# Kernel tuning notes

Measured on AMD Instinct MI355X. Metric: run time of the kernel, lower is better.

Reference implementation:

```python
import jax, jax.numpy as jnp
import numpy as np

B, T, C = 8, 2048, 1024
HEAD_SIZE = 64
HEAD_NUM = 0
NUM_HEADS = 16


def setup_inputs() -> dict:
    key = jax.random.key(0)
    k1, k2, k3, k4 = jax.random.split(key, 4)
    x = jax.random.normal(k1, (B, T, C), dtype=jnp.float32)
    s = C ** -0.5  # Linear init scale
    Wq = jax.random.normal(k2, (C, HEAD_SIZE), dtype=jnp.float32) * s
    Wk = jax.random.normal(k3, (C, HEAD_SIZE), dtype=jnp.float32) * s
    Wv = jax.random.normal(k4, (C, HEAD_SIZE), dtype=jnp.float32) * s
    return {"x": x, "Wq": Wq, "Wk": Wk, "Wv": Wv}


def reference(x, Wq, Wk, Wv):
    # single head of self-attention with ALiBi bias + causal mask (dropout in eval mode = identity)
    q = x @ Wq  # [B,T,H]
    k = x @ Wk  # [B,T,H]
    v = x @ Wv  # [B,T,H]
    scale = jnp.float32(HEAD_SIZE) ** -0.5
    t = jnp.arange(T)
    # base_bias[i,j] = j - i, scaled by per-head ALiBi slope
    slope = 2.0 ** (-8.0 * (HEAD_NUM + 1) / NUM_HEADS)
    m = (t[None, :] - t[:, None]).astype(jnp.float32) * slope  # [T,T]
    # note: bias is added BEFORE the 1/sqrt(d) scaling, as in the original
    scores = (jnp.einsum('bqh,bkh->bqk', q, k) + m) * scale  # [B,T,T]
    causal = t[None, :] <= t[:, None]  # [T,T] lower-triangular
    scores = jnp.where(causal, scores, -jnp.inf)
    attn = jax.nn.softmax(scores, axis=-1)
    out = jnp.einsum('bqk,bkh->bqh', attn, v)  # [B,T,H]
    return out
```

## Files before the change

### kernel.cpp

```cpp
#include <hip/hip_runtime.h>
#include <hip/hip_bf16.h>
#include <math.h>

#define B_ 8
#define T_ 2048
#define C_ 1024
#define H_ 64
#define M_ (B_*T_)

typedef __attribute__((ext_vector_type(8))) short bf16x8;
typedef __attribute__((ext_vector_type(4))) float floatx4;

static __device__ __forceinline__ unsigned short f2bf(float f) {
    union { float f; unsigned u; } v; v.f = f;
    unsigned r = v.u + 0x7fffu + ((v.u >> 16) & 1u);
    return (unsigned short)(r >> 16);
}
static __device__ __forceinline__ unsigned short f2bf_fast(float f) {
    union { float f; unsigned u; } v; v.f = f;
    return (unsigned short)((v.u + 0x8000u) >> 16);
}
static __device__ __forceinline__ unsigned pk2h(float lo, float hi) {
    union { float f; unsigned u; } a, b; a.f = lo; b.f = hi;
    return __builtin_amdgcn_perm(b.u + 0x8000u, a.u + 0x8000u, 0x07060302u);
}
static __device__ __forceinline__ bf16x8 cvt8(float4 f0, float4 f1) {
    union { uint4 u; bf16x8 v; } r;
    r.u.x = pk2h(f0.x, f0.y); r.u.y = pk2h(f0.z, f0.w);
    r.u.z = pk2h(f1.x, f1.y); r.u.w = pk2h(f1.z, f1.w);
    return r.v;
}

#define MFMA(a,b,c) __builtin_amdgcn_mfma_f32_16x16x32_bf16((a),(b),(c),0,0,0)

__global__ __launch_bounds__(256) void wprep_kernel(
    const float* __restrict__ Wq, const float* __restrict__ Wk,
    const float* __restrict__ Wv, unsigned short* __restrict__ wt2)
{
    const int f    = blockIdx.x * 256 + threadIdx.x;
    const int nt   = f >> 11;
    const int kc   = (f >> 6) & 31;
    const int lane = f & 63;
    const int l15  = lane & 15, quad = lane >> 4;
    const int col  = nt * 16 + l15;
    const float* W = (col < 64) ? Wq : ((col < 128) ? Wk : Wv);
    const int   cw = col & 63;
    const float sc = (col < 64) ? 0.125f : 1.0f;
    unsigned short o[8];
    #pragma unroll
    for (int j = 0; j < 8; j++) {
        const int kk = kc * 32 + quad * 8 + j;
        o[j] = f2bf(W[(size_t)kk * 64 + cw] * sc);
    }
    *(uint4*)&wt2[(size_t)f * 8] = *(const uint4*)o;
}

__global__ __launch_bounds__(256) void qkv_kernel(
    const float* __restrict__ x, const unsigned short* __restrict__ wt2,
    unsigned short* __restrict__ qo, unsigned short* __restrict__ ko,
    unsigned short* __restrict__ vo)
{
    __shared__ __align__(16) unsigned short smem[64 * 200];
    #define XS_(buf) (smem + (buf) * 4608)

    const int t    = threadIdx.x;
    const int w    = t >> 6;
    const int lane = t & 63;
    const int l15  = lane & 15;
    const int quad = lane >> 4;
    const int r0   = blockIdx.x * 64;

    const int srow = t >> 2;
    const int g0   = t & 3;
    const float* xrow = x + (size_t)(r0 + srow) * C_;

    const unsigned short* wb = wt2 + (size_t)(w * 3) * 32 * 512 + lane * 8;

    floatx4 acc[4][3];
    #pragma unroll
    for (int mt = 0; mt < 4; mt++)
        #pragma unroll
        for (int nt = 0; nt < 3; nt++) acc[mt][nt] = (floatx4)(0.0f);

    float4 xA[4], xB[4];
    bf16x8 wcur[6], wnxt[6];

    #pragma unroll
    for (int j = 0; j < 2; j++) {
        const int g = g0 + 4 * j;
        xA[2*j+0] = *(const float4*)(xrow + g * 8);
        xA[2*j+1] = *(const float4*)(xrow + g * 8 + 4);
        xB[2*j+0] = *(const float4*)(xrow + 64 + g * 8);
        xB[2*j+1] = *(const float4*)(xrow + 64 + g * 8 + 4);
    }
    #pragma unroll
    for (int nt = 0; nt < 3; nt++)
        #pragma unroll
        for (int ks = 0; ks < 2; ks++)
            wcur[nt * 2 + ks] = *(const bf16x8*)(wb + (size_t)(nt * 32 + ks) * 512);
    #pragma unroll
    for (int j = 0; j < 2; j++) {
        const int g = g0 + 4 * j;
        *(bf16x8*)(XS_(0) + srow * 72 + g * 8) = cvt8(xA[2*j], xA[2*j+1]);
    }
    __syncthreads();

    #define QSTEP(c, Xcur, Xnext, buf)                                         \
    {                                                                          \
        if ((c) < 14) {                                                        \
            const int k2 = ((c) + 2) * 64;                                     \
            _Pragma("unroll")                                                  \
            for (int j = 0; j < 2; j++) {                                      \
                const int g = g0 + 4 * j;                                      \
                Xcur[2*j+0] = *(const float4*)(xrow + k2 + g * 8);             \
                Xcur[2*j+1] = *(const float4*)(xrow + k2 + g * 8 + 4);         \
            }                                                                  \
        }                                                                      \
        if ((c) < 15) {                                                        \
            _Pragma("unroll")                                                  \
            for (int nt = 0; nt < 3; nt++)                                     \
                _Pragma("unroll")                                              \
                for (int ks = 0; ks < 2; ks++)                                 \
                    wnxt[nt * 2 + ks] = *(const bf16x8*)                       \
                        (wb + (size_t)(nt * 32 + 2 * ((c) + 1) + ks) * 512);   \
        }                                                                      \
        _Pragma("unroll")                                                      \
        for (int ks = 0; ks < 2; ks++) {                                       \
            bf16x8 af[4];                                                      \
            _Pragma("unroll")                                                  \
            for (int mt = 0; mt < 4; mt++)                                     \
                af[mt] = *(const bf16x8*)                                      \
                    (XS_(buf) + (mt * 16 + l15) * 72 + ks * 32 + quad * 8);    \
            _Pragma("unroll")                                                  \
            for (int mt = 0; mt < 4; mt++)                                     \
                _Pragma("unroll")                                              \
                for (int nt = 0; nt < 3; nt++)                                 \
                    acc[mt][nt] = MFMA(af[mt], wcur[nt * 2 + ks], acc[mt][nt]);\
        }                                                                      \
        if ((c) < 15) {                                                        \
            _Pragma("unroll")                                                  \
            for (int j = 0; j < 2; j++) {                                      \
                const int g = g0 + 4 * j;                                      \
                *(bf16x8*)(XS_((buf) ^ 1) + srow * 72 + g * 8)                 \
                    = cvt8(Xnext[2*j], Xnext[2*j+1]);                          \
            }                                                                  \
            _Pragma("unroll")                                                  \
            for (int i = 0; i < 6; i++) wcur[i] = wnxt[i];                     \
        }                                                                      \
        __syncthreads();                                                       \
    }

    for (int cc = 0; cc < 16; cc += 2) {
        QSTEP(cc,     xA, xB, 0)
        QSTEP(cc + 1, xB, xA, 1)
    }
    #undef QSTEP

    #pragma unroll
    for (int mt = 0; mt < 4; mt++)
        #pragma unroll
        for (int nt = 0; nt < 3; nt++) {
            const int col = w * 48 + nt * 16 + l15;
            #pragma unroll
            for (int r = 0; r < 4; r++)
                smem[(mt * 16 + quad * 4 + r) * 200 + col] = f2bf(acc[mt][nt][r]);
        }
    __syncthreads();

    {
        #pragma unroll
        for (int i = 0; i < 2; i++) {
            const int fo  = t + i * 256;
            const int row = fo >> 3;
            const int oct = fo & 7;
            *(uint4*)&qo[(size_t)(r0 + row) * 64 + oct * 8] =
                *(const uint4*)&smem[row * 200 + oct * 8];
            *(uint4*)&ko[(size_t)(r0 + row) * 64 + oct * 8] =
                *(const uint4*)&smem[row * 200 + 64 + oct * 8];
        }
    }
    {
        const int h = t >> 2, ts = (t & 3) * 16;
        const int bb = r0 >> 11, tt = r0 & 2047;
        unsigned short tmp[16];
        #pragma unroll
        for (int j = 0; j < 16; j++) tmp[j] = smem[(ts + j) * 200 + 128 + h];
        #pragma unroll
        for (int j = 0; j < 2; j++)
            *(uint4*)&vo[((size_t)bb * 64 + h) * 2048 + tt + ts + j * 8] =
                *(uint4*)&tmp[j * 8];
    }
    #undef XS_
}

__global__ __launch_bounds__(256, 2) void attn_kernel(
    const unsigned short* __restrict__ q,
    const unsigned short* __restrict__ k,
    const unsigned short* __restrict__ vT,
    float* __restrict__ out)
{
    __shared__ __align__(16) unsigned char smem[32768 + 1024];
    unsigned short* pT  = (unsigned short*)smem;
    float*          Omg = (float*)smem;
    float*          mlg = (float*)(smem + 32768);

    const int t    = threadIdx.x;
    const int w    = t >> 6;
    const int lane = t & 63;
    const int l15  = lane & 15;
    const int quad = lane >> 4;
    const int b    = blockIdx.x & 7;
    const int qt   = 63 - (blockIdx.x >> 3);
    const int q0   = qt * 32;
    const size_t kb = (size_t)b * T_ * 64;

    bf16x8 qf[2][2];
    #pragma unroll
    for (int rt = 0; rt < 2; rt++)
        #pragma unroll
        for (int ks = 0; ks < 2; ks++)
            qf[rt][ks] = *(const bf16x8*)
                &q[kb + (size_t)(q0 + rt * 16 + l15) * 64 + ks * 32 + quad * 8];

    floatx4 O[2][4];
    float mrow[2][4], lrow[2][4], igb[2][4];
    const float bs = 0.088388347648318447f;
    #pragma unroll
    for (int rt = 0; rt < 2; rt++) {
        #pragma unroll
        for (int nt = 0; nt < 4; nt++) O[rt][nt] = (floatx4)(0.0f);
        #pragma unroll
        for (int r = 0; r < 4; r++) {
            mrow[rt][r] = -INFINITY; lrow[rt][r] = 0.0f;
            igb[rt][r] = (float)(q0 + rt * 16 + quad * 4 + r) * bs;
        }
    }

    const int nsteps = (q0 + 32 + 63) >> 6;
    const int ns4    = (nsteps + 3) >> 2;
    const int sBeg   = w * ns4;
    const int sEnd   = min(sBeg + ns4, nsteps);
    unsigned short* pw = pT + w * 32 * 72;

    bf16x8 kf[4][2], vf[4][2];
    #define LOADK(dK, jj0)                                                     \
        { _Pragma("unroll")                                                    \
          for (int nt = 0; nt < 4; nt++)                                       \
              _Pragma("unroll")                                                \
              for (int ks = 0; ks < 2; ks++)                                   \
                  dK[nt][ks] = *(const bf16x8*)                                \
                      &k[kb + (size_t)((jj0) + nt*16 + l15)*64 + ks*32 + quad*8]; }
    #define LOADV(dV, jj0)                                                     \
        { _Pragma("unroll")                                                    \
          for (int nt = 0; nt < 4; nt++)                                       \
              _Pragma("unroll")                                                \
              for (int ks = 0; ks < 2; ks++)                                   \
                  dV[nt][ks] = *(const bf16x8*)                                \
                      &vT[((size_t)b*64 + nt*16 + l15)*2048 + (jj0) + ks*32 + quad*8]; }

    if (sBeg < sEnd) LOADK(kf, sBeg * 64)

    for (int s = sBeg; s < sEnd; s++) {
        const int j0 = s * 64;

        floatx4 sc[2][4];
        #pragma unroll
        for (int rt = 0; rt < 2; rt++)
            #pragma unroll
            for (int nt = 0; nt < 4; nt++) {
                floatx4 z = (floatx4)(0.0f);
                z = MFMA(qf[rt][0], kf[nt][0], z);
                z = MFMA(qf[rt][1], kf[nt][1], z);
                sc[rt][nt] = z;
            }

        LOADV(vf, j0)
        bf16x8 kf2[4][2];
        const bool more = (s + 1 < sEnd);
        if (more) LOADK(kf2, (s + 1) * 64)

        const float jbase = (float)(j0 + l15) * bs;
        #pragma unroll
        for (int rt = 0; rt < 2; rt++)
            #pragma unroll
            for (int r = 0; r < 4; r++) {
                const int   ig = q0 + rt * 16 + quad * 4 + r;
                const float c0 = jbase - igb[rt][r];
                float xv[4];
                float mloc = -INFINITY;
                #pragma unroll
                for (int nt = 0; nt < 4; nt++) {
                    const int j = j0 + nt * 16 + l15;
                    float v2 = (sc[rt][nt][r] + c0) + (float)(nt * 16) * bs;
                    if (j > ig) v2 = -INFINITY;
                    xv[nt] = v2;
                    mloc = fmaxf(mloc, v2);
                }
                #pragma unroll
                for (int off = 1; off < 16; off <<= 1)
                    mloc = fmaxf(mloc, __shfl_xor(mloc, off));
                const float mnew = fmaxf(mrow[rt][r], mloc);
                const float mq   = (mnew == -INFINITY) ? 0.0f : mnew;
                const float alpha = __expf(mrow[rt][r] - mq);
                mrow[rt][r] = mnew;
                float ps = 0.0f;
                #pragma unroll
                for (int nt = 0; nt < 4; nt++) {
                    const float p = __expf(xv[nt] - mq);
                    ps += p;
                    pw[(rt * 16 + quad * 4 + r) * 72 + nt * 16 + l15] = f2bf_fast(p);
                }
                lrow[rt][r] = lrow[rt][r] * alpha + ps;
                #pragma unroll
                for (int nt = 0; nt < 4; nt++) O[rt][nt][r] *= alpha;
            }

        #pragma unroll
        for (int rt = 0; rt < 2; rt++) {
            const bf16x8 pf0 = *(const bf16x8*)&pw[(rt * 16 + l15) * 72 + quad * 8];
            const bf16x8 pf1 = *(const bf16x8*)&pw[(rt * 16 + l15) * 72 + 32 + quad * 8];
            #pragma unroll
            for (int nt = 0; nt < 4; nt++) {
                O[rt][nt] = MFMA(pf0, vf[nt][0], O[rt][nt]);
                O[rt][nt] = MFMA(pf1, vf[nt][1], O[rt][nt]);
            }
        }

        if (more) {
            #pragma unroll
            for (int nt = 0; nt < 4; nt++)
                #pragma unroll
                for (int ks = 0; ks < 2; ks++)
                    kf[nt][ks] = kf2[nt][ks];
        }
    }
    #undef LOADK
    #undef LOADV

    #pragma unroll
    for (int rt = 0; rt < 2; rt++)
        #pragma unroll
        for (int r = 0; r < 4; r++)
            #pragma unroll
            for (int off = 1; off < 16; off <<= 1)
                lrow[rt][r] += __shfl_xor(lrow[rt][r], off);

    __syncthreads();

    #pragma unroll
    for (int rt = 0; rt < 2; rt++)
        #pragma unroll
        for (int nt = 0; nt < 4; nt++)
            #pragma unroll
            for (int r = 0; r < 4; r++)
                Omg[w * 2048 + (rt * 16 + quad * 4 + r) * 64 + nt * 16 + l15]
                    = O[rt][nt][r];
    if (l15 == 0) {
        #pragma unroll
        for (int rt = 0; rt < 2; rt++)
            #pragma unroll
            for (int r = 0; r < 4; r++) {
                mlg[w * 64 + rt * 16 + quad * 4 + r]      = mrow[rt][r];
                mlg[w * 64 + 32 + rt * 16 + quad * 4 + r] = lrow[rt][r];
            }
    }
    __syncthreads();

    {
        const int row = t >> 3;
        const int hq  = (t & 7) << 3;
        float mstar = -INFINITY;
        #pragma unroll
        for (int w2 = 0; w2 < 4; w2++)
            mstar = fmaxf(mstar, mlg[w2 * 64 + row]);
        floatx4 oa0 = (floatx4)(0.0f), oa1 = (floatx4)(0.0f);
        float lsum = 0.0f;
        #pragma unroll
        for (int w2 = 0; w2 < 4; w2++) {
            const float wg = __expf(mlg[w2 * 64 + row] - mstar);
            lsum += wg * mlg[w2 * 64 + 32 + row];
            oa0 += wg * *(const floatx4*)&Omg[w2 * 2048 + row * 64 + hq];
            oa1 += wg * *(const floatx4*)&Omg[w2 * 2048 + row * 64 + hq + 4];
        }
        const float inv = 1.0f / lsum;
        *(floatx4*)&out[kb + (size_t)(q0 + row) * 64 + hq]     = oa0 * inv;
        *(floatx4*)&out[kb + (size_t)(q0 + row) * 64 + hq + 4] = oa1 * inv;
    }
}

extern "C" void kernel_launch(void* const* d_in, const int* in_sizes, int n_in,
                              void* d_out, int out_size, void* d_ws, size_t ws_size,
                              hipStream_t stream) {
    (void)in_sizes; (void)n_in; (void)out_size; (void)ws_size;
    const float* x  = (const float*)d_in[0];
    const float* Wq = (const float*)d_in[1];
    const float* Wk = (const float*)d_in[2];
    const float* Wv = (const float*)d_in[3];
    float* out = (float*)d_out;

    unsigned short* wt2 = (unsigned short*)d_ws;
    unsigned short* qw  = wt2 + 196608;
    unsigned short* kw  = qw + (size_t)M_ * H_;
    unsigned short* vw  = kw + (size_t)M_ * H_;

    wprep_kernel<<<96, 256, 0, stream>>>(Wq, Wk, Wv, wt2);
    qkv_kernel<<<M_ / 64, 256, 0, stream>>>(x, wt2, qw, kw, vw);
    attn_kernel<<<B_ * 64, 256, 0, stream>>>(qw, kw, vw, out);
}
```

Before: 139.4 us.

## Halve QKV row tile and switch attention softmax to exp2 with diagonal-only masking

New measurement: 137.3 us. About the same (-1.5%).

```diff
diff --git a/kernel.cpp b/kernel.cpp
--- a/kernel.cpp
+++ b/kernel.cpp
@@ -29,6 +29,17 @@
     r.u.x = pk2h(f0.x, f0.y); r.u.y = pk2h(f0.z, f0.w);
     r.u.z = pk2h(f1.x, f1.y); r.u.w = pk2h(f1.z, f1.w);
     return r.v;
+}
+static __device__ __forceinline__ float fexp2(float x) {
+#if defined(__has_builtin)
+#if __has_builtin(__builtin_amdgcn_exp2f)
+    return __builtin_amdgcn_exp2f(x);
+#else
+    return exp2f(x);
+#endif
+#else
+    return exp2f(x);
+#endif
 }
 
 #define MFMA(a,b,c) __builtin_amdgcn_mfma_f32_16x16x32_bf16((a),(b),(c),0,0,0)
@@ -60,61 +71,49 @@
     unsigned short* __restrict__ qo, unsigned short* __restrict__ ko,
     unsigned short* __restrict__ vo)
 {
-    __shared__ __align__(16) unsigned short smem[64 * 200];
-    #define XS_(buf) (smem + (buf) * 4608)
+    __shared__ __align__(16) unsigned short smem[32 * 200];
+    #define XS_(buf) (smem + (buf) * 2304)
 
     const int t    = threadIdx.x;
     const int w    = t >> 6;
     const int lane = t & 63;
     const int l15  = lane & 15;
     const int quad = lane >> 4;
-    const int r0   = blockIdx.x * 64;
-
-    const int srow = t >> 2;
-    const int g0   = t & 3;
+    const int r0   = blockIdx.x * 32;
+
+    const int srow = t >> 3;
+    const int g0   = t & 7;
     const float* xrow = x + (size_t)(r0 + srow) * C_;
 
     const unsigned short* wb = wt2 + (size_t)(w * 3) * 32 * 512 + lane * 8;
 
-    floatx4 acc[4][3];
-    #pragma unroll
-    for (int mt = 0; mt < 4; mt++)
+    floatx4 acc[2][3];
+    #pragma unroll
+    for (int mt = 0; mt < 2; mt++)
         #pragma unroll
         for (int nt = 0; nt < 3; nt++) acc[mt][nt] = (floatx4)(0.0f);
 
-    float4 xA[4], xB[4];
+    float4 xA[2], xB[2];
     bf16x8 wcur[6], wnxt[6];
 
-    #pragma unroll
-    for (int j = 0; j < 2; j++) {
-        const int g = g0 + 4 * j;
-        xA[2*j+0] = *(const float4*)(xrow + g * 8);
-        xA[2*j+1] = *(const float4*)(xrow + g * 8 + 4);
-        xB[2*j+0] = *(const float4*)(xrow + 64 + g * 8);
-        xB[2*j+1] = *(const float4*)(xrow + 64 + g * 8 + 4);
-    }
+    xA[0] = *(const float4*)(xrow + g0 * 8);
+    xA[1] = *(const float4*)(xrow + g0 * 8 + 4);
+    xB[0] = *(const float4*)(xrow + 64 + g0 * 8);
+    xB[1] = *(const float4*)(xrow + 64 + g0 * 8 + 4);
     #pragma unroll
     for (int nt = 0; nt < 3; nt++)
         #pragma unroll
         for (int ks = 0; ks < 2; ks++)
             wcur[nt * 2 + ks] = *(const bf16x8*)(wb + (size_t)(nt * 32 + ks) * 512);
-    #pragma unroll
-    for (int j = 0; j < 2; j++) {
-        const int g = g0 + 4 * j;
-        *(bf16x8*)(XS_(0) + srow * 72 + g * 8) = cvt8(xA[2*j], xA[2*j+1]);
-    }
+    *(bf16x8*)(XS_(0) + srow * 72 + g0 * 8) = cvt8(xA[0], xA[1]);
     __syncthreads();
 
     #define QSTEP(c, Xcur, Xnext, buf)                                         \
     {                                                                          \
         if ((c) < 14) {                                                        \
             const int k2 = ((c) + 2) * 64;                                     \
-            _Pragma("unroll")                                                  \
-            for (int j = 0; j < 2; j++) {                                      \
-                const int g = g0 + 4 * j;                                      \
-                Xcur[2*j+0] = *(const float4*)(xrow + k2 + g * 8);             \
-                Xcur[2*j+1] = *(const float4*)(xrow + k2 + g * 8 + 4);         \
-            }                                                                  \
+            Xcur[0] = *(const float4*)(xrow + k2 + g0 * 8);                    \
+            Xcur[1] = *(const float4*)(xrow + k2 + g0 * 8 + 4);                \
         }                                                                      \
         if ((c) < 15) {                                                        \
             _Pragma("unroll")                                                  \
@@ -126,24 +125,20 @@
         }                                                                      \
         _Pragma("unroll")                                                      \
         for (int ks = 0; ks < 2; ks++) {                                       \
-            bf16x8 af[4];                                                      \
+            bf16x8 af[2];                                                      \
             _Pragma("unroll")                                                  \
-            for (int mt = 0; mt < 4; mt++)                                     \
+            for (int mt = 0; mt < 2; mt++)                                     \
                 af[mt] = *(const bf16x8*)                                      \
                     (XS_(buf) + (mt * 16 + l15) * 72 + ks * 32 + quad * 8);    \
             _Pragma("unroll")                                                  \
-            for (int mt = 0; mt < 4; mt++)                                     \
+            for (int mt = 0; mt < 2; mt++)                                     \
                 _Pragma("unroll")                                              \
                 for (int nt = 0; nt < 3; nt++)                                 \
                     acc[mt][nt] = MFMA(af[mt], wcur[nt * 2 + ks], acc[mt][nt]);\
         }                                                                      \
         if ((c) < 15) {                                                        \
-            _Pragma("unroll")                                                  \
-            for (int j = 0; j < 2; j++) {                                      \
-                const int g = g0 + 4 * j;                                      \
-                *(bf16x8*)(XS_((buf) ^ 1) + srow * 72 + g * 8)                 \
-                    = cvt8(Xnext[2*j], Xnext[2*j+1]);                          \
-            }                                                                  \
+            *(bf16x8*)(XS_((buf) ^ 1) + srow * 72 + g0 * 8)                    \
+                = cvt8(Xnext[0], Xnext[1]);                                    \
             _Pragma("unroll")                                                  \
             for (int i = 0; i < 6; i++) wcur[i] = wnxt[i];                     \
         }                                                                      \
@@ -157,7 +152,7 @@
     #undef QSTEP
 
     #pragma unroll
-    for (int mt = 0; mt < 4; mt++)
+    for (int mt = 0; mt < 2; mt++)
         #pragma unroll
         for (int nt = 0; nt < 3; nt++) {
             const int col = w * 48 + nt * 16 + l15;
@@ -168,30 +163,26 @@
     __syncthreads();
 
     {
-        #pragma unroll
-        for (int i = 0; i < 2; i++) {
-            const int fo  = t + i * 256;
-            const int row = fo >> 3;
-            const int oct = fo & 7;
-            *(uint4*)&qo[(size_t)(r0 + row) * 64 + oct * 8] =
-                *(const uint4*)&smem[row * 200 + oct * 8];
-            *(uint4*)&ko[(size_t)(r0 + row) * 64 + oct * 8] =
-                *(const uint4*)&smem[row * 200 + 64 + oct * 8];
-        }
+        const int row = t >> 3;
+        const int oct = t & 7;
+        *(uint4*)&qo[(size_t)(r0 + row) * 64 + oct * 8] =
+            *(const uint4*)&smem[row * 200 + oct * 8];
+        *(uint4*)&ko[(size_t)(r0 + row) * 64 + oct * 8] =
+            *(const uint4*)&smem[row * 200 + 64 + oct * 8];
     }
     {
-        const int h = t >> 2, ts = (t & 3) * 16;
+        const int h = t >> 2, ts = (t & 3) * 8;
         const int bb = r0 >> 11, tt = r0 & 2047;
-        unsigned short tmp[16];
-        #pragma unroll
-        for (int j = 0; j < 16; j++) tmp[j] = smem[(ts + j) * 200 + 128 + h];
-        #pragma unroll
-        for (int j = 0; j < 2; j++)
-            *(uint4*)&vo[((size_t)bb * 64 + h) * 2048 + tt + ts + j * 8] =
-                *(uint4*)&tmp[j * 8];
+        unsigned short tmp[8];
+        #pragma unroll
+        for (int j = 0; j < 8; j++) tmp[j] = smem[(ts + j) * 200 + 128 + h];
+        *(uint4*)&vo[((size_t)bb * 64 + h) * 2048 + tt + ts] = *(uint4*)&tmp[0];
     }
     #undef XS_
 }
+
+#define L2E 1.4426950408889634f
+#define BS2 0.12751743f
 
 __global__ __launch_bounds__(256, 2) void attn_kernel(
     const unsigned short* __restrict__ q,
@@ -223,17 +214,13 @@
                 &q[kb + (size_t)(q0 + rt * 16 + l15) * 64 + ks * 32 + quad * 8];
 
     floatx4 O[2][4];
-    float mrow[2][4], lrow[2][4], igb[2][4];
-    const float bs = 0.088388347648318447f;
+    float mrow[2][4], lrow[2][4];
     #pragma unroll
     for (int rt = 0; rt < 2; rt++) {
         #pragma unroll
         for (int nt = 0; nt < 4; nt++) O[rt][nt] = (floatx4)(0.0f);
         #pragma unroll
-        for (int r = 0; r < 4; r++) {
-            mrow[rt][r] = -INFINITY; lrow[rt][r] = 0.0f;
-            igb[rt][r] = (float)(q0 + rt * 16 + quad * 4 + r) * bs;
-        }
+        for (int r = 0; r < 4; r++) { mrow[rt][r] = -INFINITY; lrow[rt][r] = 0.0f; }
     }
 
     const int nsteps = (q0 + 32 + 63) >> 6;
@@ -258,6 +245,43 @@
                   dV[nt][ks] = *(const bf16x8*)                                \
                       &vT[((size_t)b*64 + nt*16 + l15)*2048 + (jj0) + ks*32 + quad*8]; }
 
+    #define SMPART(MASKED)                                                     \
+    {                                                                          \
+        _Pragma("unroll")                                                      \
+        for (int rt = 0; rt < 2; rt++)                                         \
+            _Pragma("unroll")                                                  \
+            for (int r = 0; r < 4; r++) {                                      \
+                float xv[4];                                                   \
+                _Pragma("unroll")                                              \
+                for (int nt = 0; nt < 4; nt++) {                               \
+                    float v2 = fmaf(sc[rt][nt][r], L2E, jn[nt]);               \
+                    if (MASKED) {                                              \
+                        const int ig = q0 + rt * 16 + quad * 4 + r;            \
+                        if (j0 + nt * 16 + l15 > ig) v2 = -INFINITY;           \
+                    }                                                          \
+                    xv[nt] = v2;                                               \
+                }                                                              \
+                float mloc = fmaxf(fmaxf(xv[0], xv[1]), fmaxf(xv[2], xv[3]));  \
+                _Pragma("unroll")                                              \
+                for (int off = 1; off < 16; off <<= 1)                         \
+                    mloc = fmaxf(mloc, __shfl_xor(mloc, off));                 \
+                const float mnew  = fmaxf(mrow[rt][r], mloc);                  \
+                const float alpha = fexp2(mrow[rt][r] - mnew);                 \
+                mrow[rt][r] = mnew;                                            \
+                float ps = 0.0f;                                               \
+                _Pragma("unroll")                                              \
+                for (int nt = 0; nt < 4; nt++) {                               \
+                    const float p = fexp2(xv[nt] - mnew);                      \
+                    ps += p;                                                   \
+                    pw[(rt * 16 + quad * 4 + r) * 72 + nt * 16 + l15]          \
+                        = f2bf_fast(p);                                        \
+                }                                                              \
+                lrow[rt][r] = lrow[rt][r] * alpha + ps;                        \
+                _Pragma("unroll")                                              \
+                for (int nt = 0; nt < 4; nt++) O[rt][nt][r] *= alpha;          \
+            }                                                                  \
+    }
+
     if (sBeg < sEnd) LOADK(kf, sBeg * 64)
 
     for (int s = sBeg; s < sEnd; s++) {
@@ -279,41 +303,10 @@
         const bool more = (s + 1 < sEnd);
         if (more) LOADK(kf2, (s + 1) * 64)
 
-        const float jbase = (float)(j0 + l15) * bs;
-        #pragma unroll
-        for (int rt = 0; rt < 2; rt++)
-            #pragma unroll
-            for (int r = 0; r < 4; r++) {
-                const int   ig = q0 + rt * 16 + quad * 4 + r;
-                const float c0 = jbase - igb[rt][r];
-                float xv[4];
-                float mloc = -INFINITY;
-                #pragma unroll
-                for (int nt = 0; nt < 4; nt++) {
-                    const int j = j0 + nt * 16 + l15;
-                    float v2 = (sc[rt][nt][r] + c0) + (float)(nt * 16) * bs;
-                    if (j > ig) v2 = -INFINITY;
-                    xv[nt] = v2;
-                    mloc = fmaxf(mloc, v2);
-                }
-                #pragma unroll
-                for (int off = 1; off < 16; off <<= 1)
-                    mloc = fmaxf(mloc, __shfl_xor(mloc, off));
-                const float mnew = fmaxf(mrow[rt][r], mloc);
-                const float mq   = (mnew == -INFINITY) ? 0.0f : mnew;
-                const float alpha = __expf(mrow[rt][r] - mq);
-                mrow[rt][r] = mnew;
-                float ps = 0.0f;
-                #pragma unroll
-                for (int nt = 0; nt < 4; nt++) {
-                    const float p = __expf(xv[nt] - mq);
-                    ps += p;
-                    pw[(rt * 16 + quad * 4 + r) * 72 + nt * 16 + l15] = f2bf_fast(p);
-                }
-                lrow[rt][r] = lrow[rt][r] * alpha + ps;
-                #pragma unroll
-                for (int nt = 0; nt < 4; nt++) O[rt][nt][r] *= alpha;
-            }
+        const float jb = (float)(j0 + l15) * BS2;
+        const float jn[4] = { jb, jb + 16.0f * BS2, jb + 32.0f * BS2,
+                              jb + 48.0f * BS2 };
+        if (s != nsteps - 1) SMPART(false) else SMPART(true);
 
         #pragma unroll
         for (int rt = 0; rt < 2; rt++) {
@@ -336,6 +329,7 @@
     }
     #undef LOADK
     #undef LOADV
+    #undef SMPART
 
     #pragma unroll
     for (int rt = 0; rt < 2; rt++)
@@ -377,7 +371,7 @@
         float lsum = 0.0f;
         #pragma unroll
         for (int w2 = 0; w2 < 4; w2++) {
-            const float wg = __expf(mlg[w2 * 64 + row] - mstar);
+            const float wg = fexp2(mlg[w2 * 64 + row] - mstar);
             lsum += wg * mlg[w2 * 64 + 32 + row];
             oa0 += wg * *(const floatx4*)&Omg[w2 * 2048 + row * 64 + hq];
             oa1 += wg * *(const floatx4*)&Omg[w2 * 2048 + row * 64 + hq + 4];
@@ -404,6 +398,6 @@
     unsigned short* vw  = kw + (size_t)M_ * H_;
 
     wprep_kernel<<<96, 256, 0, stream>>>(Wq, Wk, Wv, wt2);
-    qkv_kernel<<<M_ / 64, 256, 0, stream>>>(x, wt2, qw, kw, vw);
+    qkv_kernel<<<M_ / 32, 256, 0, stream>>>(x, wt2, qw, kw, vw);
     attn_kernel<<<B_ * 64, 256, 0, stream>>>(qw, kw, vw, out);
 }
```
